# Kernel optimization log

Hardware: AMD Instinct MI355X
Metric: run time of the kernel (lower is better)

Reference implementation:

```python
import jax, jax.numpy as jnp
import numpy as np

B, S, F = 8, 2048, 256
NUM_HEADS, HEAD_DIM = 8, 64
PROJ = NUM_HEADS * HEAD_DIM


def setup_inputs() -> dict:
    key = jax.random.key(0)
    ks = jax.random.split(key, 5)
    scale = 1.0 / np.sqrt(F)
    return {
        "x": jax.random.normal(ks[0], (B, S, F), dtype=jnp.float32),
        "Wq": jax.random.normal(ks[1], (F, PROJ), dtype=jnp.float32) * scale,
        "Wk": jax.random.normal(ks[2], (F, PROJ), dtype=jnp.float32) * scale,
        "Wv": jax.random.normal(ks[3], (F, PROJ), dtype=jnp.float32) * scale,
        "Wo": jax.random.normal(ks[4], (PROJ, F), dtype=jnp.float32) * (1.0 / np.sqrt(PROJ)),
        "bo": jnp.zeros((F,), dtype=jnp.float32),
    }


def _split_heads(t):
    # [B, S, PROJ] -> [B, H, S, D]
    b, s, _ = t.shape
    return t.reshape(b, s, NUM_HEADS, HEAD_DIM).transpose(0, 2, 1, 3)


def reference(x, Wq, Wk, Wv, Wo, bo):
    q = _split_heads(x @ Wq)  # [B,H,S,D]
    k = _split_heads(x @ Wk)
    v = _split_heads(x @ Wv)

    scale = jnp.sqrt(jnp.asarray(HEAD_DIM, dtype=x.dtype))
    score = jnp.einsum("bhqd,bhkd->bhqk", q, k) / scale  # [B,H,S,S]

    # additive causal mask: -1e9 above the diagonal (matches tf band_part trick)
    s = x.shape[1]
    neg = (1.0 - jnp.tril(jnp.ones((s, s), dtype=x.dtype))) * -1e9
    score = score + neg[None, None, :, :]

    weights = jax.nn.softmax(score, axis=-1)
    attn = jnp.einsum("bhqk,bhkd->bhqd", weights, v)  # [B,H,S,D]
    concat = attn.transpose(0, 2, 1, 3).reshape(x.shape[0], s, PROJ)
    out = concat @ Wo + bo  # [B,S,F]
    return out[:, -1, :]  # keep only last sequence position
```

## Files before the change

### kernel.cpp

```cpp
#include <hip/hip_runtime.h>

#define BB 8
#define SS 2048
#define FF 256
#define HH 8
#define DD 64
#define PROJ 512
#define NCHUNK 32
#define CHUNK (SS / NCHUNK)

__global__ void k_qr(const float* __restrict__ x, const float* __restrict__ Wq,
                     const float* __restrict__ Wk, float* __restrict__ r) {
    const int b = blockIdx.x / HH;
    const int h = blockIdx.x % HH;
    __shared__ float xrow[FF];
    __shared__ float qp[4][DD];
    __shared__ float qh[DD];
    const int t = threadIdx.x;

    xrow[t] = x[((size_t)b * SS + (SS - 1)) * FF + t];
    __syncthreads();

    {
        const int g = t >> 6, d = t & 63;
        float acc = 0.f;
        const float* wqp = Wq + (size_t)(g * 64) * PROJ + h * DD + d;
#pragma unroll 8
        for (int j = 0; j < 64; ++j)
            acc += xrow[g * 64 + j] * wqp[(size_t)j * PROJ];
        qp[g][d] = acc;
    }
    __syncthreads();
    if (t < DD) qh[t] = qp[0][t] + qp[1][t] + qp[2][t] + qp[3][t];
    __syncthreads();

    const float4* wk4 = reinterpret_cast<const float4*>(Wk + (size_t)t * PROJ + h * DD);
    float acc = 0.f;
#pragma unroll
    for (int d4 = 0; d4 < DD / 4; ++d4) {
        float4 w = wk4[d4];
        acc += w.x * qh[d4 * 4 + 0] + w.y * qh[d4 * 4 + 1] +
               w.z * qh[d4 * 4 + 2] + w.w * qh[d4 * 4 + 3];
    }
    r[(size_t)blockIdx.x * FF + t] = acc * 0.125f;
}

__global__ void k_fa(const float* __restrict__ x, const float* __restrict__ r,
                     float* __restrict__ ycp, float* __restrict__ ml) {
    const int b = blockIdx.x / NCHUNK;
    const int c = blockIdx.x % NCHUNK;
    const int t = threadIdx.x;
    __shared__ float rl[HH][FF + 4];
    __shared__ float es[HH][CHUNK + 4];
    __shared__ float yp[2][HH][FF];

    for (int i = t; i < HH * FF; i += 512)
        rl[i >> 8][i & 255] = r[(size_t)b * HH * FF + i];
    __syncthreads();

    {
        const int sl = t >> 3, h = t & 7;
        const float4* xp =
            reinterpret_cast<const float4*>(x + ((size_t)b * SS + c * CHUNK + sl) * FF);
        const float* rp = rl[h];
        float acc = 0.f;
#pragma unroll 8
        for (int f4 = 0; f4 < FF / 4; ++f4) {
            float4 xv = xp[f4];
            acc += xv.x * rp[f4 * 4 + 0] + xv.y * rp[f4 * 4 + 1] +
                   xv.z * rp[f4 * 4 + 2] + xv.w * rp[f4 * 4 + 3];
        }
        es[h][sl] = acc;
    }
    __syncthreads();

    {
        const int h = t >> 6, ln = t & 63;
        float v = es[h][ln];
        float m = v;
#pragma unroll
        for (int off = 32; off; off >>= 1) m = fmaxf(m, __shfl_xor(m, off));
        float e = __expf(v - m);
        float l = e;
#pragma unroll
        for (int off = 32; off; off >>= 1) l += __shfl_xor(l, off);
        es[h][ln] = e;
        if (ln == 0) {
            float* mlp = ml + ((size_t)(b * NCHUNK + c)) * 2 * HH;
            mlp[h] = m;
            mlp[HH + h] = l;
        }
    }
    __syncthreads();

    {
        const int f = t & 255, half = t >> 8;
        float acc[HH] = {0, 0, 0, 0, 0, 0, 0, 0};
        const float* xp = x + ((size_t)b * SS + c * CHUNK + half * 32) * FF + f;
        for (int s = 0; s < 32; ++s) {
            const float xv = xp[(size_t)s * FF];
            const int sl = half * 32 + s;
#pragma unroll
            for (int h = 0; h < HH; ++h) acc[h] += es[h][sl] * xv;
        }
#pragma unroll
        for (int h = 0; h < HH; ++h) yp[half][h][f] = acc[h];
    }
    __syncthreads();

    for (int i = t; i < HH * FF; i += 512) {
        const int h = i >> 8, f = i & 255;
        ycp[((size_t)(b * NCHUNK + c) * HH + h) * FF + f] = yp[0][h][f] + yp[1][h][f];
    }
}

__global__ void k_comb(const float* __restrict__ ycp, const float* __restrict__ ml,
                       const float* __restrict__ Wv, float* __restrict__ attn_g) {
    const int b = blockIdx.x / HH;
    const int h = blockIdx.x % HH;
    const int t = threadIdx.x;
    __shared__ float alpha[NCHUNK];
    __shared__ float Ls;
    __shared__ float yt[FF];
    __shared__ float atl[4][DD];

    if (t < 64) {
        const int ln = t;
        const float* mlp = ml + ((size_t)(b * NCHUNK + (ln & 31))) * 2 * HH;
        float m = (ln < NCHUNK) ? mlp[h] : -1e30f;
        float M = m;
#pragma unroll
        for (int off = 32; off; off >>= 1) M = fmaxf(M, __shfl_xor(M, off));
        float a = (ln < NCHUNK) ? __expf(m - M) : 0.f;
        float lw = (ln < NCHUNK) ? a * mlp[HH + h] : 0.f;
#pragma unroll
        for (int off = 32; off; off >>= 1) lw += __shfl_xor(lw, off);
        if (ln < NCHUNK) alpha[ln] = a;
        if (ln == 0) Ls = lw;
    }
    __syncthreads();

    {
        float acc = 0.f;
        const float* yp = ycp + ((size_t)(b * NCHUNK) * HH + h) * FF + t;
#pragma unroll 8
        for (int c = 0; c < NCHUNK; ++c)
            acc += alpha[c] * yp[(size_t)c * HH * FF];
        yt[t] = acc;
    }
    __syncthreads();

    {
        const int q = t >> 6, d = t & 63;
        float acc = 0.f;
        const float* wvp = Wv + (size_t)(q * 64) * PROJ + h * DD + d;
#pragma unroll 8
        for (int j = 0; j < 64; ++j)
            acc += yt[q * 64 + j] * wvp[(size_t)j * PROJ];
        atl[q][d] = acc;
    }
    __syncthreads();

    if (t < DD) {
        attn_g[(size_t)b * PROJ + h * DD + t] =
            (atl[0][t] + atl[1][t] + atl[2][t] + atl[3][t]) / Ls;
    }
}

__global__ void k_out2(const float* __restrict__ attn_g, const float* __restrict__ Wo,
                       const float* __restrict__ bo, float* __restrict__ out) {
    const int b = blockIdx.x;
    const int t = threadIdx.x;
    __shared__ float al[PROJ];
    __shared__ float po[4][FF];

    if (t < PROJ) al[t] = attn_g[(size_t)b * PROJ + t];
    __syncthreads();

    {
        const int f = t & 255, sl = t >> 8;
        float acc = 0.f;
        const float* wop = Wo + (size_t)(sl * 128) * FF + f;
        const float* ap = al + sl * 128;
#pragma unroll 8
        for (int j = 0; j < 128; ++j)
            acc += ap[j] * wop[(size_t)j * FF];
        po[sl][f] = acc;
    }
    __syncthreads();

    if (t < FF)
        out[(size_t)b * FF + t] = bo[t] + po[0][t] + po[1][t] + po[2][t] + po[3][t];
}

extern "C" void kernel_launch(void* const* d_in, const int* in_sizes, int n_in,
                              void* d_out, int out_size, void* d_ws, size_t ws_size,
                              hipStream_t stream) {
    const float* x  = (const float*)d_in[0];
    const float* Wq = (const float*)d_in[1];
    const float* Wk = (const float*)d_in[2];
    const float* Wv = (const float*)d_in[3];
    const float* Wo = (const float*)d_in[4];
    const float* bo = (const float*)d_in[5];
    float* out = (float*)d_out;

    float* ws     = (float*)d_ws;
    float* r      = ws;
    float* ycp    = r + BB * HH * FF;
    float* ml     = ycp + (size_t)BB * NCHUNK * HH * FF;
    float* attn_g = ml + BB * NCHUNK * 2 * HH;

    k_qr<<<BB * HH, 256, 0, stream>>>(x, Wq, Wk, r);
    k_fa<<<BB * NCHUNK, 512, 0, stream>>>(x, r, ycp, ml);
    k_comb<<<BB * HH, 256, 0, stream>>>(ycp, ml, Wv, attn_g);
    k_out2<<<BB, 1024, 0, stream>>>(attn_g, Wo, bo, out);
}
```

Before: 34.43 us.

## Fuse four attention stages into one cooperative kernel with grid syncs

```diff
diff --git a/kernel.cpp b/kernel.cpp
--- a/kernel.cpp
+++ b/kernel.cpp
@@ -1,4 +1,7 @@
 #include <hip/hip_runtime.h>
+#include <hip/hip_cooperative_groups.h>
+
+namespace cg = cooperative_groups;
 
 #define BB 8
 #define SS 2048
@@ -9,188 +12,212 @@
 #define NCHUNK 32
 #define CHUNK (SS / NCHUNK)
 
-__global__ void k_qr(const float* __restrict__ x, const float* __restrict__ Wq,
-                     const float* __restrict__ Wk, float* __restrict__ r) {
-    const int b = blockIdx.x / HH;
-    const int h = blockIdx.x % HH;
-    __shared__ float xrow[FF];
-    __shared__ float qp[4][DD];
-    __shared__ float qh[DD];
-    const int t = threadIdx.x;
-
-    xrow[t] = x[((size_t)b * SS + (SS - 1)) * FF + t];
-    __syncthreads();
-
-    {
-        const int g = t >> 6, d = t & 63;
-        float acc = 0.f;
-        const float* wqp = Wq + (size_t)(g * 64) * PROJ + h * DD + d;
-#pragma unroll 8
-        for (int j = 0; j < 64; ++j)
-            acc += xrow[g * 64 + j] * wqp[(size_t)j * PROJ];
-        qp[g][d] = acc;
-    }
-    __syncthreads();
-    if (t < DD) qh[t] = qp[0][t] + qp[1][t] + qp[2][t] + qp[3][t];
-    __syncthreads();
-
-    const float4* wk4 = reinterpret_cast<const float4*>(Wk + (size_t)t * PROJ + h * DD);
-    float acc = 0.f;
-#pragma unroll
-    for (int d4 = 0; d4 < DD / 4; ++d4) {
-        float4 w = wk4[d4];
-        acc += w.x * qh[d4 * 4 + 0] + w.y * qh[d4 * 4 + 1] +
-               w.z * qh[d4 * 4 + 2] + w.w * qh[d4 * 4 + 3];
-    }
-    r[(size_t)blockIdx.x * FF + t] = acc * 0.125f;
-}
-
-__global__ void k_fa(const float* __restrict__ x, const float* __restrict__ r,
-                     float* __restrict__ ycp, float* __restrict__ ml) {
-    const int b = blockIdx.x / NCHUNK;
-    const int c = blockIdx.x % NCHUNK;
-    const int t = threadIdx.x;
+__global__ void __launch_bounds__(512) k_fused(
+    const float* __restrict__ x, const float* __restrict__ Wq,
+    const float* __restrict__ Wk, const float* __restrict__ Wv,
+    const float* __restrict__ Wo, const float* __restrict__ bo,
+    float* __restrict__ out, float* __restrict__ ws)
+{
+    float* r      = ws;
+    float* ycp    = r + BB * HH * FF;
+    float* ml     = ycp + (size_t)BB * NCHUNK * HH * FF;
+    float* attn_g = ml + BB * NCHUNK * 2 * HH;
+
+    cg::grid_group grid = cg::this_grid();
+    const int blk = blockIdx.x;
+    const int t   = threadIdx.x;
+
     __shared__ float rl[HH][FF + 4];
     __shared__ float es[HH][CHUNK + 4];
     __shared__ float yp[2][HH][FF];
 
-    for (int i = t; i < HH * FF; i += 512)
-        rl[i >> 8][i & 255] = r[(size_t)b * HH * FF + i];
-    __syncthreads();
+    float* xrow = &yp[0][0][0];
+    float (*qp)[DD] = (float (*)[DD])&yp[1][0][0];
+    float* esf = &es[0][0];
+
+    if (blk < BB * HH) {
+        const int b = blk / HH, h = blk % HH;
+        if (t < FF) xrow[t] = x[((size_t)b * SS + (SS - 1)) * FF + t];
+        __syncthreads();
+
+        {
+            const int g = t >> 6, d = t & 63;
+            float acc = 0.f;
+            const float* wqp = Wq + (size_t)(g * 32) * PROJ + h * DD + d;
+#pragma unroll 8
+            for (int j = 0; j < 32; ++j)
+                acc += xrow[g * 32 + j] * wqp[(size_t)j * PROJ];
+            qp[g][d] = acc;
+        }
+        __syncthreads();
+        if (t < DD) {
+            float q = 0.f;
+#pragma unroll
+            for (int g = 0; g < 8; ++g) q += qp[g][t];
+            esf[t] = q;
+        }
+        __syncthreads();
+
+        if (t < FF) {
+            const float4* wk4 =
+                reinterpret_cast<const float4*>(Wk + (size_t)t * PROJ + h * DD);
+            float acc = 0.f;
+#pragma unroll
+            for (int d4 = 0; d4 < DD / 4; ++d4) {
+                float4 w = wk4[d4];
+                acc += w.x * esf[d4 * 4 + 0] + w.y * esf[d4 * 4 + 1] +
+                       w.z * esf[d4 * 4 + 2] + w.w * esf[d4 * 4 + 3];
+            }
+            r[(size_t)blk * FF + t] = acc * 0.125f;
+        }
+    }
+    grid.sync();
 
     {
-        const int sl = t >> 3, h = t & 7;
-        const float4* xp =
-            reinterpret_cast<const float4*>(x + ((size_t)b * SS + c * CHUNK + sl) * FF);
-        const float* rp = rl[h];
-        float acc = 0.f;
-#pragma unroll 8
-        for (int f4 = 0; f4 < FF / 4; ++f4) {
-            float4 xv = xp[f4];
-            acc += xv.x * rp[f4 * 4 + 0] + xv.y * rp[f4 * 4 + 1] +
-                   xv.z * rp[f4 * 4 + 2] + xv.w * rp[f4 * 4 + 3];
-        }
-        es[h][sl] = acc;
-    }
-    __syncthreads();
-
-    {
-        const int h = t >> 6, ln = t & 63;
-        float v = es[h][ln];
-        float m = v;
-#pragma unroll
-        for (int off = 32; off; off >>= 1) m = fmaxf(m, __shfl_xor(m, off));
-        float e = __expf(v - m);
-        float l = e;
-#pragma unroll
-        for (int off = 32; off; off >>= 1) l += __shfl_xor(l, off);
-        es[h][ln] = e;
-        if (ln == 0) {
-            float* mlp = ml + ((size_t)(b * NCHUNK + c)) * 2 * HH;
-            mlp[h] = m;
-            mlp[HH + h] = l;
-        }
-    }
-    __syncthreads();
-
-    {
-        const int f = t & 255, half = t >> 8;
-        float acc[HH] = {0, 0, 0, 0, 0, 0, 0, 0};
-        const float* xp = x + ((size_t)b * SS + c * CHUNK + half * 32) * FF + f;
-        for (int s = 0; s < 32; ++s) {
-            const float xv = xp[(size_t)s * FF];
-            const int sl = half * 32 + s;
-#pragma unroll
-            for (int h = 0; h < HH; ++h) acc[h] += es[h][sl] * xv;
-        }
-#pragma unroll
-        for (int h = 0; h < HH; ++h) yp[half][h][f] = acc[h];
-    }
-    __syncthreads();
-
-    for (int i = t; i < HH * FF; i += 512) {
-        const int h = i >> 8, f = i & 255;
-        ycp[((size_t)(b * NCHUNK + c) * HH + h) * FF + f] = yp[0][h][f] + yp[1][h][f];
-    }
-}
-
-__global__ void k_comb(const float* __restrict__ ycp, const float* __restrict__ ml,
-                       const float* __restrict__ Wv, float* __restrict__ attn_g) {
-    const int b = blockIdx.x / HH;
-    const int h = blockIdx.x % HH;
-    const int t = threadIdx.x;
-    __shared__ float alpha[NCHUNK];
-    __shared__ float Ls;
-    __shared__ float yt[FF];
-    __shared__ float atl[4][DD];
-
-    if (t < 64) {
-        const int ln = t;
-        const float* mlp = ml + ((size_t)(b * NCHUNK + (ln & 31))) * 2 * HH;
-        float m = (ln < NCHUNK) ? mlp[h] : -1e30f;
-        float M = m;
-#pragma unroll
-        for (int off = 32; off; off >>= 1) M = fmaxf(M, __shfl_xor(M, off));
-        float a = (ln < NCHUNK) ? __expf(m - M) : 0.f;
-        float lw = (ln < NCHUNK) ? a * mlp[HH + h] : 0.f;
-#pragma unroll
-        for (int off = 32; off; off >>= 1) lw += __shfl_xor(lw, off);
-        if (ln < NCHUNK) alpha[ln] = a;
-        if (ln == 0) Ls = lw;
-    }
-    __syncthreads();
-
-    {
-        float acc = 0.f;
-        const float* yp = ycp + ((size_t)(b * NCHUNK) * HH + h) * FF + t;
-#pragma unroll 8
-        for (int c = 0; c < NCHUNK; ++c)
-            acc += alpha[c] * yp[(size_t)c * HH * FF];
-        yt[t] = acc;
-    }
-    __syncthreads();
-
-    {
-        const int q = t >> 6, d = t & 63;
-        float acc = 0.f;
-        const float* wvp = Wv + (size_t)(q * 64) * PROJ + h * DD + d;
-#pragma unroll 8
-        for (int j = 0; j < 64; ++j)
-            acc += yt[q * 64 + j] * wvp[(size_t)j * PROJ];
-        atl[q][d] = acc;
-    }
-    __syncthreads();
-
-    if (t < DD) {
-        attn_g[(size_t)b * PROJ + h * DD + t] =
-            (atl[0][t] + atl[1][t] + atl[2][t] + atl[3][t]) / Ls;
-    }
-}
-
-__global__ void k_out2(const float* __restrict__ attn_g, const float* __restrict__ Wo,
-                       const float* __restrict__ bo, float* __restrict__ out) {
-    const int b = blockIdx.x;
-    const int t = threadIdx.x;
-    __shared__ float al[PROJ];
-    __shared__ float po[4][FF];
-
-    if (t < PROJ) al[t] = attn_g[(size_t)b * PROJ + t];
-    __syncthreads();
-
-    {
-        const int f = t & 255, sl = t >> 8;
-        float acc = 0.f;
-        const float* wop = Wo + (size_t)(sl * 128) * FF + f;
-        const float* ap = al + sl * 128;
-#pragma unroll 8
-        for (int j = 0; j < 128; ++j)
-            acc += ap[j] * wop[(size_t)j * FF];
-        po[sl][f] = acc;
-    }
-    __syncthreads();
-
-    if (t < FF)
-        out[(size_t)b * FF + t] = bo[t] + po[0][t] + po[1][t] + po[2][t] + po[3][t];
+        const int b = blk / NCHUNK, c = blk % NCHUNK;
+
+        for (int i = t; i < HH * FF; i += 512)
+            rl[i >> 8][i & 255] = r[(size_t)b * HH * FF + i];
+        __syncthreads();
+
+        {
+            const int sl = t >> 3, h = t & 7;
+            const float4* xp = reinterpret_cast<const float4*>(
+                x + ((size_t)b * SS + c * CHUNK + sl) * FF);
+            const float* rp = rl[h];
+            float acc = 0.f;
+#pragma unroll 8
+            for (int f4 = 0; f4 < FF / 4; ++f4) {
+                float4 xv = xp[f4];
+                acc += xv.x * rp[f4 * 4 + 0] + xv.y * rp[f4 * 4 + 1] +
+                       xv.z * rp[f4 * 4 + 2] + xv.w * rp[f4 * 4 + 3];
+            }
+            es[h][sl] = acc;
+        }
+        __syncthreads();
+
+        {
+            const int h = t >> 6, ln = t & 63;
+            float v = es[h][ln];
+            float m = v;
+#pragma unroll
+            for (int off = 32; off; off >>= 1) m = fmaxf(m, __shfl_xor(m, off));
+            float e = __expf(v - m);
+            float l = e;
+#pragma unroll
+            for (int off = 32; off; off >>= 1) l += __shfl_xor(l, off);
+            es[h][ln] = e;
+            if (ln == 0) {
+                float* mlp = ml + ((size_t)(b * NCHUNK + c)) * 2 * HH;
+                mlp[h] = m;
+                mlp[HH + h] = l;
+            }
+        }
+        __syncthreads();
+
+        {
+            const int f = t & 255, half = t >> 8;
+            float acc[HH] = {0, 0, 0, 0, 0, 0, 0, 0};
+            const float* xp = x + ((size_t)b * SS + c * CHUNK + half * 32) * FF + f;
+            for (int s = 0; s < 32; ++s) {
+                const float xv = xp[(size_t)s * FF];
+                const int sl = half * 32 + s;
+#pragma unroll
+                for (int h = 0; h < HH; ++h) acc[h] += es[h][sl] * xv;
+            }
+#pragma unroll
+            for (int h = 0; h < HH; ++h) yp[half][h][f] = acc[h];
+        }
+        __syncthreads();
+
+        for (int i = t; i < HH * FF; i += 512) {
+            const int h = i >> 8, f = i & 255;
+            ycp[((size_t)(b * NCHUNK + c) * HH + h) * FF + f] =
+                yp[0][h][f] + yp[1][h][f];
+        }
+    }
+    grid.sync();
+
+    if (blk < BB * HH) {
+        const int b = blk / HH, h = blk % HH;
+        float* alpha = esf;
+        float* Lsp   = esf + 40;
+
+        if (t < 64) {
+            const int ln = t;
+            const float* mlp = ml + ((size_t)(b * NCHUNK + (ln & 31))) * 2 * HH;
+            float m = (ln < NCHUNK) ? mlp[h] : -1e30f;
+            float M = m;
+#pragma unroll
+            for (int off = 32; off; off >>= 1) M = fmaxf(M, __shfl_xor(M, off));
+            float a  = (ln < NCHUNK) ? __expf(m - M) : 0.f;
+            float lw = (ln < NCHUNK) ? a * mlp[HH + h] : 0.f;
+#pragma unroll
+            for (int off = 32; off; off >>= 1) lw += __shfl_xor(lw, off);
+            if (ln < NCHUNK) alpha[ln] = a;
+            if (ln == 0) *Lsp = lw;
+        }
+        __syncthreads();
+
+        float* yt = xrow;
+        if (t < FF) {
+            float acc = 0.f;
+            const float* ypg = ycp + ((size_t)(b * NCHUNK) * HH + h) * FF + t;
+#pragma unroll 8
+            for (int c = 0; c < NCHUNK; ++c)
+                acc += alpha[c] * ypg[(size_t)c * HH * FF];
+            yt[t] = acc;
+        }
+        __syncthreads();
+
+        float (*atl)[DD] = qp;
+        {
+            const int q8 = t >> 6, d = t & 63;
+            float acc = 0.f;
+            const float* wvp = Wv + (size_t)(q8 * 32) * PROJ + h * DD + d;
+#pragma unroll 8
+            for (int j = 0; j < 32; ++j)
+                acc += yt[q8 * 32 + j] * wvp[(size_t)j * PROJ];
+            atl[q8][d] = acc;
+        }
+        __syncthreads();
+
+        if (t < DD) {
+            float acc = 0.f;
+#pragma unroll
+            for (int q8 = 0; q8 < 8; ++q8) acc += atl[q8][t];
+            attn_g[(size_t)b * PROJ + h * DD + t] = acc / *Lsp;
+        }
+    }
+    grid.sync();
+
+    if (blk < BB * 4) {
+        const int b = blk >> 2, fs = blk & 3;
+        float* al = &rl[0][0];
+        float (*po)[DD] = qp;
+
+        if (t < PROJ) al[t] = attn_g[(size_t)b * PROJ + t];
+        __syncthreads();
+
+        {
+            const int sl = t >> 6, fl = t & 63;
+            float acc = 0.f;
+            const float* wop = Wo + (size_t)(sl * 64) * FF + fs * 64 + fl;
+            const float* ap = al + sl * 64;
+#pragma unroll 8
+            for (int j = 0; j < 64; ++j)
+                acc += ap[j] * wop[(size_t)j * FF];
+            po[sl][fl] = acc;
+        }
+        __syncthreads();
+
+        if (t < DD) {
+            float acc = bo[fs * 64 + t];
+#pragma unroll
+            for (int sl = 0; sl < 8; ++sl) acc += po[sl][t];
+            out[(size_t)b * FF + fs * 64 + t] = acc;
+        }
+    }
 }
 
 extern "C" void kernel_launch(void* const* d_in, const int* in_sizes, int n_in,
@@ -203,15 +230,10 @@
     const float* Wo = (const float*)d_in[4];
     const float* bo = (const float*)d_in[5];
     float* out = (float*)d_out;
-
-    float* ws     = (float*)d_ws;
-    float* r      = ws;
-    float* ycp    = r + BB * HH * FF;
-    float* ml     = ycp + (size_t)BB * NCHUNK * HH * FF;
-    float* attn_g = ml + BB * NCHUNK * 2 * HH;
-
-    k_qr<<<BB * HH, 256, 0, stream>>>(x, Wq, Wk, r);
-    k_fa<<<BB * NCHUNK, 512, 0, stream>>>(x, r, ycp, ml);
-    k_comb<<<BB * HH, 256, 0, stream>>>(ycp, ml, Wv, attn_g);
-    k_out2<<<BB, 1024, 0, stream>>>(attn_g, Wo, bo, out);
+    float* wsf = (float*)d_ws;
+
+    void* args[] = {(void*)&x, (void*)&Wq, (void*)&Wk, (void*)&Wv,
+                    (void*)&Wo, (void*)&bo, (void*)&out, (void*)&wsf};
+    hipLaunchCooperativeKernel((const void*)k_fused, dim3(BB * NCHUNK), dim3(512),
+                               args, 0, stream);
 }
```

Result: slower. 116.5 us (+238.5%).

## Fold chunk combine into attention kernel and precompute Wv·Wo product

Applied to the files above, without the earlier changes.

```diff
diff --git a/kernel.cpp b/kernel.cpp
--- a/kernel.cpp
+++ b/kernel.cpp
@@ -10,13 +10,16 @@
 #define CHUNK (SS / NCHUNK)
 
 __global__ void k_qr(const float* __restrict__ x, const float* __restrict__ Wq,
-                     const float* __restrict__ Wk, float* __restrict__ r) {
+                     const float* __restrict__ Wk, float* __restrict__ r,
+                     unsigned int* __restrict__ done) {
     const int b = blockIdx.x / HH;
     const int h = blockIdx.x % HH;
+    const int t = threadIdx.x;
     __shared__ float xrow[FF];
     __shared__ float qp[4][DD];
     __shared__ float qh[DD];
-    const int t = threadIdx.x;
+
+    if (blockIdx.x == 0 && t < BB) done[t] = 0u;
 
     xrow[t] = x[((size_t)b * SS + (SS - 1)) * FF + t];
     __syncthreads();
@@ -45,14 +48,50 @@
     r[(size_t)blockIdx.x * FF + t] = acc * 0.125f;
 }
 
-__global__ void k_fa(const float* __restrict__ x, const float* __restrict__ r,
-                     float* __restrict__ ycp, float* __restrict__ ml) {
-    const int b = blockIdx.x / NCHUNK;
-    const int c = blockIdx.x % NCHUNK;
+__global__ void __launch_bounds__(512) k_megaZ(
+    const float* __restrict__ x, const float* __restrict__ r,
+    const float* __restrict__ Wv, const float* __restrict__ Wo,
+    float* __restrict__ ycp, float* __restrict__ ml,
+    float* __restrict__ yn, float* __restrict__ Z,
+    unsigned int* __restrict__ done) {
+    const int blk = blockIdx.x;
     const int t = threadIdx.x;
     __shared__ float rl[HH][FF + 4];
     __shared__ float es[HH][CHUNK + 4];
     __shared__ float yp[2][HH][FF];
+    __shared__ int is_last;
+
+    if (blk >= BB * NCHUNK) {
+        const int zi = blk - BB * NCHUNK;
+        const int h = zi >> 4, ct = zi & 15;
+        float (*wos)[16] = (float (*)[16])&yp[0][0][0];
+        for (int i = t; i < DD * 16; i += 512) {
+            const int d = i >> 4, j = i & 15;
+            wos[d][j] = Wo[(size_t)(h * DD + d) * FF + ct * 16 + j];
+        }
+        __syncthreads();
+        const int rr = t & 255, ch = t >> 8;
+        float acc[8] = {0, 0, 0, 0, 0, 0, 0, 0};
+        const float4* wv4 =
+            reinterpret_cast<const float4*>(Wv + (size_t)rr * PROJ + h * DD);
+#pragma unroll
+        for (int d4 = 0; d4 < 16; ++d4) {
+            float4 wv = wv4[d4];
+#pragma unroll
+            for (int jj = 0; jj < 8; ++jj) {
+                acc[jj] += wv.x * wos[d4 * 4 + 0][ch * 8 + jj] +
+                           wv.y * wos[d4 * 4 + 1][ch * 8 + jj] +
+                           wv.z * wos[d4 * 4 + 2][ch * 8 + jj] +
+                           wv.w * wos[d4 * 4 + 3][ch * 8 + jj];
+            }
+        }
+        float* zp = Z + ((size_t)(h * FF + rr)) * FF + ct * 16 + ch * 8;
+#pragma unroll
+        for (int jj = 0; jj < 8; ++jj) zp[jj] = acc[jj];
+        return;
+    }
+
+    const int b = blk / NCHUNK, c = blk % NCHUNK;
 
     for (int i = t; i < HH * FF; i += 512)
         rl[i >> 8][i & 255] = r[(size_t)b * HH * FF + i];
@@ -60,8 +99,8 @@
 
     {
         const int sl = t >> 3, h = t & 7;
-        const float4* xp =
-            reinterpret_cast<const float4*>(x + ((size_t)b * SS + c * CHUNK + sl) * FF);
+        const float4* xp = reinterpret_cast<const float4*>(
+            x + ((size_t)b * SS + c * CHUNK + sl) * FF);
         const float* rp = rl[h];
         float acc = 0.f;
 #pragma unroll 8
@@ -110,87 +149,77 @@
 
     for (int i = t; i < HH * FF; i += 512) {
         const int h = i >> 8, f = i & 255;
-        ycp[((size_t)(b * NCHUNK + c) * HH + h) * FF + f] = yp[0][h][f] + yp[1][h][f];
-    }
-}
-
-__global__ void k_comb(const float* __restrict__ ycp, const float* __restrict__ ml,
-                       const float* __restrict__ Wv, float* __restrict__ attn_g) {
-    const int b = blockIdx.x / HH;
-    const int h = blockIdx.x % HH;
-    const int t = threadIdx.x;
-    __shared__ float alpha[NCHUNK];
-    __shared__ float Ls;
-    __shared__ float yt[FF];
-    __shared__ float atl[4][DD];
-
-    if (t < 64) {
-        const int ln = t;
-        const float* mlp = ml + ((size_t)(b * NCHUNK + (ln & 31))) * 2 * HH;
-        float m = (ln < NCHUNK) ? mlp[h] : -1e30f;
+        ycp[((size_t)(b * NCHUNK + c) * HH + h) * FF + f] =
+            yp[0][h][f] + yp[1][h][f];
+    }
+
+    __syncthreads();
+    if (t == 0) {
+        __threadfence();
+        unsigned int old = atomicAdd(&done[b], 1u);
+        is_last = (old == NCHUNK - 1) ? 1 : 0;
+    }
+    __syncthreads();
+    if (!is_last) return;
+    if (t == 0) __threadfence();
+    __syncthreads();
+
+    {
+        const int th = t >> 6, ln = t & 63;
+        const float* mlb = ml + (size_t)(b * NCHUNK) * 2 * HH;
+        float m = (ln < NCHUNK) ? mlb[ln * 2 * HH + th] : -1e30f;
         float M = m;
 #pragma unroll
         for (int off = 32; off; off >>= 1) M = fmaxf(M, __shfl_xor(M, off));
         float a = (ln < NCHUNK) ? __expf(m - M) : 0.f;
-        float lw = (ln < NCHUNK) ? a * mlp[HH + h] : 0.f;
+        float lw = (ln < NCHUNK) ? a * mlb[ln * 2 * HH + HH + th] : 0.f;
 #pragma unroll
         for (int off = 32; off; off >>= 1) lw += __shfl_xor(lw, off);
-        if (ln < NCHUNK) alpha[ln] = a;
-        if (ln == 0) Ls = lw;
-    }
-    __syncthreads();
-
-    {
-        float acc = 0.f;
-        const float* yp = ycp + ((size_t)(b * NCHUNK) * HH + h) * FF + t;
+        if (ln < NCHUNK) es[th][ln] = a;
+        if (ln == 0) es[th][32] = 1.f / lw;
+    }
+    __syncthreads();
+
+    for (int i = t; i < HH * FF; i += 512) {
+        const int h = i >> 8, f = i & 255;
+        const float* yb = ycp + ((size_t)(b * NCHUNK) * HH + h) * FF + f;
+        float acc = 0.f;
 #pragma unroll 8
         for (int c = 0; c < NCHUNK; ++c)
-            acc += alpha[c] * yp[(size_t)c * HH * FF];
-        yt[t] = acc;
-    }
-    __syncthreads();
-
-    {
-        const int q = t >> 6, d = t & 63;
-        float acc = 0.f;
-        const float* wvp = Wv + (size_t)(q * 64) * PROJ + h * DD + d;
-#pragma unroll 8
-        for (int j = 0; j < 64; ++j)
-            acc += yt[q * 64 + j] * wvp[(size_t)j * PROJ];
-        atl[q][d] = acc;
-    }
-    __syncthreads();
-
-    if (t < DD) {
-        attn_g[(size_t)b * PROJ + h * DD + t] =
-            (atl[0][t] + atl[1][t] + atl[2][t] + atl[3][t]) / Ls;
-    }
-}
-
-__global__ void k_out2(const float* __restrict__ attn_g, const float* __restrict__ Wo,
+            acc += es[h][c] * yb[(size_t)c * HH * FF];
+        yn[(size_t)b * (HH * FF) + i] = acc * es[h][32];
+    }
+}
+
+__global__ void k_out3(const float* __restrict__ yn, const float* __restrict__ Z,
                        const float* __restrict__ bo, float* __restrict__ out) {
-    const int b = blockIdx.x;
+    const int b = blockIdx.x >> 3;
+    const int fs = blockIdx.x & 7;
     const int t = threadIdx.x;
-    __shared__ float al[PROJ];
-    __shared__ float po[4][FF];
-
-    if (t < PROJ) al[t] = attn_g[(size_t)b * PROJ + t];
-    __syncthreads();
-
-    {
-        const int f = t & 255, sl = t >> 8;
-        float acc = 0.f;
-        const float* wop = Wo + (size_t)(sl * 128) * FF + f;
-        const float* ap = al + sl * 128;
-#pragma unroll 8
-        for (int j = 0; j < 128; ++j)
-            acc += ap[j] * wop[(size_t)j * FF];
-        po[sl][f] = acc;
-    }
-    __syncthreads();
-
-    if (t < FF)
-        out[(size_t)b * FF + t] = bo[t] + po[0][t] + po[1][t] + po[2][t] + po[3][t];
+    __shared__ float ys[HH * FF];
+    __shared__ float po[8][32];
+
+    for (int i = t; i < HH * FF; i += 256) ys[i] = yn[(size_t)b * HH * FF + i];
+    __syncthreads();
+
+    const int j = t & 31, g = t >> 5;
+    {
+        float acc = 0.f;
+        const float* zp = Z + ((size_t)g * 256) * FF + fs * 32 + j;
+        const float* yg = ys + g * 256;
+#pragma unroll 8
+        for (int rr = 0; rr < 256; ++rr)
+            acc += yg[rr] * zp[(size_t)rr * FF];
+        po[g][j] = acc;
+    }
+    __syncthreads();
+
+    if (t < 32) {
+        float o = bo[fs * 32 + t];
+#pragma unroll
+        for (int g2 = 0; g2 < 8; ++g2) o += po[g2][t];
+        out[(size_t)b * FF + fs * 32 + t] = o;
+    }
 }
 
 extern "C" void kernel_launch(void* const* d_in, const int* in_sizes, int n_in,
@@ -204,14 +233,15 @@
     const float* bo = (const float*)d_in[5];
     float* out = (float*)d_out;
 
-    float* ws     = (float*)d_ws;
-    float* r      = ws;
-    float* ycp    = r + BB * HH * FF;
-    float* ml     = ycp + (size_t)BB * NCHUNK * HH * FF;
-    float* attn_g = ml + BB * NCHUNK * 2 * HH;
-
-    k_qr<<<BB * HH, 256, 0, stream>>>(x, Wq, Wk, r);
-    k_fa<<<BB * NCHUNK, 512, 0, stream>>>(x, r, ycp, ml);
-    k_comb<<<BB * HH, 256, 0, stream>>>(ycp, ml, Wv, attn_g);
-    k_out2<<<BB, 1024, 0, stream>>>(attn_g, Wo, bo, out);
-}
+    float* ws  = (float*)d_ws;
+    float* r   = ws;
+    float* ycp = r + BB * HH * FF;
+    float* ml  = ycp + (size_t)BB * NCHUNK * HH * FF;
+    float* yn  = ml + BB * NCHUNK * 2 * HH;
+    float* Z   = yn + BB * HH * FF;
+    unsigned int* done = (unsigned int*)(Z + (size_t)HH * FF * FF);
+
+    k_qr<<<BB * HH, 256, 0, stream>>>(x, Wq, Wk, r, done);
+    k_megaZ<<<BB * NCHUNK + 128, 512, 0, stream>>>(x, r, Wv, Wo, ycp, ml, yn, Z, done);
+    k_out3<<<BB * 8, 256, 0, stream>>>(yn, Z, bo, out);
+}
```

Result: slower. 57.54 us (+67.1%).
